# Performance work log

Measured on AMD Instinct MI355X. Metric: run time of the kernel, lower is better.

Reference implementation:

```python
import jax, jax.numpy as jnp
from jax import lax
import numpy as np

HEAD_DIM = 64

def _conv(x, w, stride, pad, groups=1):
    return lax.conv_general_dilated(x, w, (stride, stride), ((pad, pad), (pad, pad)),
                                    dimension_numbers=('NCHW', 'OIHW', 'NCHW'),
                                    feature_group_count=groups)

def _conv_transpose(x, w, b, stride=2, pad=1):
    # PyTorch ConvTranspose2d weight layout is [in, out, kh, kw]
    wf = jnp.transpose(w, (1, 0, 2, 3))[:, :, ::-1, ::-1]
    p = w.shape[2] - 1 - pad
    y = lax.conv_general_dilated(x, wf, (1, 1), ((p, p), (p, p)),
                                 lhs_dilation=(stride, stride),
                                 dimension_numbers=('NCHW', 'OIHW', 'NCHW'))
    return y + b[None, :, None, None]

def _bn(x, g, b, m, v):
    s = g / jnp.sqrt(v + 1e-5)
    return x * s[None, :, None, None] + (b - m * s)[None, :, None, None]

def _relu6(x):
    return jnp.clip(x, 0.0, 6.0)

def reference(x, down_w, down_b, up_w, up_b, coarse_qkv_w, coarse_qkv_b,
              topk_qkv_w, topk_qkv_b, dw_w, bn1_g, bn1_b, bn1_m, bn1_v,
              pw_w, bn2_g, bn2_b, bn2_m, bn2_v):
    hd = HEAD_DIM
    # ---- CoarseSelfAttention ----
    xd = _conv(x, down_w, 2, 1) + down_b[None, :, None, None]   # [B,C,h,w]
    B, C, h, w = xd.shape
    nh = C // hd
    t = xd.reshape(B, nh, hd, h * w).transpose(0, 1, 3, 2)      # [B,nh,hw,hd]
    qkv = t @ coarse_qkv_w.T + coarse_qkv_b
    q, k, v = jnp.split(qkv, 3, axis=-1)
    attn = jax.nn.softmax(jnp.einsum('bnid,bnjd->bnij', k, q), axis=-1)  # k @ q^T (unscaled, as in source)
    coarse_score = attn.sum(axis=-2)                            # [B,nh,hw]
    K = (h * w) // 4
    _, top_k = lax.top_k(coarse_score, K)                       # [B,nh,K]
    out = jnp.einsum('bnij,bnjd->bnid', attn, v)
    out = out.transpose(0, 1, 3, 2).reshape(B, C, h, w)
    coarse_out = _conv_transpose(out, up_w, up_b)               # [B,C,H,W]

    # ---- TopkSelfAttention ----
    H, W = coarse_out.shape[2], coarse_out.shape[3]
    P = (H // 2) * (W // 2)
    xh = coarse_out.reshape(B, nh, hd, H, W)
    # unfold(3,2,2).unfold(4,2,2) -> [B,nh,hd,H/2,W/2,2,2] -> [B,nh,hd,P,2,2]
    patches = xh.reshape(B, nh, hd, H // 2, 2, W // 2, 2).transpose(0, 1, 2, 3, 5, 4, 6)
    patches = patches.reshape(B, nh, hd, P, 2, 2)
    idx = jnp.broadcast_to(top_k[:, :, None, :, None, None], (B, nh, hd, K, 2, 2))
    gathered = jnp.take_along_axis(patches, idx, axis=3)        # [B,nh,hd,K,2,2]
    tokens = gathered.reshape(B, nh, hd, K * 4).transpose(0, 1, 3, 2)  # [B,nh,4K,hd]
    qkv2 = tokens @ topk_qkv_w.T + topk_qkv_b
    q2, k2, v2 = jnp.split(qkv2, 3, axis=-1)
    attn2 = jax.nn.softmax(jnp.einsum('bnid,bnjd->bnij', k2, q2), axis=-1)
    out2 = jnp.einsum('bnij,bnjd->bnid', attn2, v2)             # [B,nh,4K,hd]
    out2 = out2.transpose(0, 1, 3, 2).reshape(B, nh, hd, K, 2, 2)
    bi = jnp.arange(B)[:, None, None]
    hi = jnp.arange(nh)[None, :, None]
    # scatter-add attended patches back into residual patches
    res = patches.at[bi, hi, :, top_k].add(out2.transpose(0, 1, 3, 2, 4, 5))
    # faithful to torch's reshape(batch, -1, patch*2, patch*2) (row-major flatten)
    region = res.reshape(B, C, H, W)

    # ---- residual add + DWConv ----
    y = coarse_out + region
    y = _relu6(_bn(_conv(y, dw_w, 1, 1, groups=C), bn1_g, bn1_b, bn1_m, bn1_v))
    y = _relu6(_bn(_conv(y, pw_w, 1, 0), bn2_g, bn2_b, bn2_m, bn2_v))
    return y

def setup_inputs() -> dict:
    key = jax.random.key(0)
    ks = jax.random.split(key, 20)
    B, C, H, W = 8, 256, 64, 64
    hd = HEAD_DIM
    s = 0.02
    n = jax.random.normal
    inp = {
        'x': n(ks[0], (B, C, H, W), dtype=jnp.float32),
        'down_w': n(ks[1], (C, C, 4, 4), dtype=jnp.float32) * s,
        'down_b': n(ks[2], (C,), dtype=jnp.float32) * s,
        'up_w': n(ks[3], (C, C, 4, 4), dtype=jnp.float32) * s,  # [in,out,kh,kw]
        'up_b': n(ks[4], (C,), dtype=jnp.float32) * s,
        'coarse_qkv_w': n(ks[5], (3 * hd, hd), dtype=jnp.float32) * s,
        'coarse_qkv_b': n(ks[6], (3 * hd,), dtype=jnp.float32) * s,
        'topk_qkv_w': n(ks[7], (3 * hd, hd), dtype=jnp.float32) * s,
        'topk_qkv_b': n(ks[8], (3 * hd,), dtype=jnp.float32) * s,
        'dw_w': n(ks[9], (C, 1, 3, 3), dtype=jnp.float32) * s,
        'bn1_g': 1.0 + n(ks[10], (C,), dtype=jnp.float32) * 0.1,
        'bn1_b': n(ks[11], (C,), dtype=jnp.float32) * 0.1,
        'bn1_m': n(ks[12], (C,), dtype=jnp.float32) * 0.1,
        'bn1_v': jax.random.uniform(ks[13], (C,), dtype=jnp.float32, minval=0.5, maxval=1.5),
        'pw_w': n(ks[14], (C, C, 1, 1), dtype=jnp.float32) * s,
        'bn2_g': 1.0 + n(ks[15], (C,), dtype=jnp.float32) * 0.1,
        'bn2_b': n(ks[16], (C,), dtype=jnp.float32) * 0.1,
        'bn2_m': n(ks[17], (C,), dtype=jnp.float32) * 0.1,
        'bn2_v': jax.random.uniform(ks[18], (C,), dtype=jnp.float32, minval=0.5, maxval=1.5),
    }
    return inp
```

## Files before the change

### kernel.cpp

```cpp
#include <hip/hip_runtime.h>

typedef short short8 __attribute__((ext_vector_type(8)));
typedef float f32x4 __attribute__((ext_vector_type(4)));

__device__ inline unsigned short f32_to_bf16_rne(float f) {
  unsigned int u = __float_as_uint(f);
  unsigned int r = (u + 0x7fffu + ((u >> 16) & 1u)) >> 16;
  return (unsigned short)r;
}
__device__ inline float bf16_to_f32(unsigned short h) {
  return __uint_as_float(((unsigned int)h) << 16);
}

constexpr size_t OFF_XD    = 0;
constexpr size_t OFF_Q     = 2097152;
constexpr size_t OFF_K     = 4194304;
constexpr size_t OFF_V     = 6291456;
constexpr size_t OFF_ATT   = 8388608;
constexpr size_t OFF_SPART = 10485760;
constexpr size_t OFF_SCORE = 14680064;
constexpr size_t OFF_IDX   = 14712832;
constexpr size_t OFF_COUT  = 14721024;
constexpr size_t OFF_Y     = 23109632;
constexpr size_t OFF_T1    = 31498240;
constexpr size_t WS_FLOATS = 39886848;

__global__ __launch_bounds__(256) void k_x2bf(const float* __restrict__ x,
    unsigned short* __restrict__ xbh, unsigned short* __restrict__ xbl) {
  int bid = blockIdx.x;
  int b = bid >> 7;
  int ih = (bid >> 1) & 63;
  int iwh = bid & 1;
  int t = threadIdx.x;
  __shared__ float ts[256][33];
  for (int it = 0; it < 32; ++it) {
    int idx = it * 256 + t;
    int ci = idx >> 5;
    int iwl = idx & 31;
    ts[ci][iwl] = x[(((size_t)(b * 256 + ci) * 64 + ih) * 64) + iwh * 32 + iwl];
  }
  __syncthreads();
  int iwl = t >> 3;
  int cb = (t & 7) * 32;
  size_t base = (((size_t)(b * 64 + ih) * 64) + iwh * 32 + iwl) * 256 + cb;
#pragma unroll
  for (int j = 0; j < 32; j += 2) {
    float v0 = ts[cb + j][iwl];
    float v1 = ts[cb + j + 1][iwl];
    unsigned short h0 = f32_to_bf16_rne(v0);
    unsigned short h1 = f32_to_bf16_rne(v1);
    unsigned short l0 = f32_to_bf16_rne(v0 - bf16_to_f32(h0));
    unsigned short l1 = f32_to_bf16_rne(v1 - bf16_to_f32(h1));
    *(ushort2*)&xbh[base + j] = make_ushort2(h0, h1);
    *(ushort2*)&xbl[base + j] = make_ushort2(l0, l1);
  }
}

__global__ __launch_bounds__(256) void k_wt_dnb(const float* __restrict__ w,
    unsigned short* __restrict__ dwhi, unsigned short* __restrict__ dwlo) {
  int idx = blockIdx.x * 256 + threadIdx.x;
  int ci = idx & 255;
  int co = (idx >> 8) & 255;
  int kk = idx >> 16;
  float v = w[((size_t)(co * 256 + ci)) * 16 + kk];
  unsigned short h = f32_to_bf16_rne(v);
  unsigned short l = f32_to_bf16_rne(v - bf16_to_f32(h));
  dwhi[idx] = h;
  dwlo[idx] = l;
}

__global__ __launch_bounds__(256) void k_wt_upb(const float* __restrict__ w,
    unsigned short* __restrict__ whi, unsigned short* __restrict__ wlo) {
  int idx = blockIdx.x * 256 + threadIdx.x;
  int ci = idx & 255;
  int co = (idx >> 8) & 255;
  int tp = idx >> 16;
  int cls = tp >> 2, tap = tp & 3;
  int r = cls >> 1, s = cls & 1;
  int a_ = tap >> 1, b_ = tap & 1;
  int kh = a_ ? (r ? 2 : 3) : (r ? 0 : 1);
  int kw = b_ ? (s ? 2 : 3) : (s ? 0 : 1);
  float v = w[((size_t)(ci * 256 + co)) * 16 + kh * 4 + kw];
  unsigned short h = f32_to_bf16_rne(v);
  unsigned short l = f32_to_bf16_rne(v - bf16_to_f32(h));
  whi[idx] = h;
  wlo[idx] = l;
}

__global__ __launch_bounds__(256) void k_conv_down_mfma(
    const unsigned short* __restrict__ xbh, const unsigned short* __restrict__ xbl,
    const unsigned short* __restrict__ dwhi, const unsigned short* __restrict__ dwlo,
    const float* __restrict__ bias, float* __restrict__ part) {
  int blk = blockIdx.x;
  int pt = blk & 31;
  int ct = (blk >> 5) & 3;
  int b = (blk >> 7) & 7;
  int ks = blk >> 10;
  int oh2 = pt >> 1;
  int owh = pt & 1;
  int tid = threadIdx.x;
  int w = tid >> 6;
  int lane = tid & 63;
  int lq = lane >> 4;
  int lr = lane & 15;
  int co = ct * 64 + w * 16 + lr;

  __shared__ __align__(16) unsigned short AH[6][34][40];
  __shared__ __align__(16) unsigned short AL[6][34][40];

  f32x4 acc[2];
  acc[0] = (f32x4){0.f, 0.f, 0.f, 0.f};
  acc[1] = (f32x4){0.f, 0.f, 0.f, 0.f};

  int ih0 = 4 * oh2 - 1;
  int iw0 = owh * 32 - 1;
  const short8 zero8 = {0, 0, 0, 0, 0, 0, 0, 0};

  for (int ch = 0; ch < 2; ++ch) {
    int ci0 = ks * 64 + ch * 32;
    __syncthreads();
    for (int idx = tid; idx < 6 * 34 * 4; idx += 256) {
      int q = idx & 3;
      int cell = idx >> 2;
      int row = cell / 34;
      int col = cell - row * 34;
      int ih = ih0 + row;
      int iw = iw0 + col;
      short8 h = zero8, l = zero8;
      if ((unsigned)ih < 64u && (unsigned)iw < 64u) {
        size_t gg = (((size_t)(b * 64 + ih) * 64) + iw) * 256 + ci0 + q * 8;
        h = *(const short8*)&xbh[gg];
        l = *(const short8*)&xbl[gg];
      }
      *(short8*)&AH[row][col][q * 8] = h;
      *(short8*)&AL[row][col][q * 8] = l;
    }
    __syncthreads();
#pragma unroll
    for (int tap = 0; tap < 16; ++tap) {
      int kh = tap >> 2, kw = tap & 3;
      size_t woff = ((size_t)tap * 256 + co) * 256 + ci0 + 8 * lq;
      short8 bh = *(const short8*)&dwhi[woff];
      short8 bl = *(const short8*)&dwlo[woff];
#pragma unroll
      for (int pf = 0; pf < 2; ++pf) {
        short8 ah = *(const short8*)&AH[2 * pf + kh][2 * lr + kw][8 * lq];
        short8 al = *(const short8*)&AL[2 * pf + kh][2 * lr + kw][8 * lq];
        acc[pf] = __builtin_amdgcn_mfma_f32_16x16x32_bf16(ah, bh, acc[pf], 0, 0, 0);
        acc[pf] = __builtin_amdgcn_mfma_f32_16x16x32_bf16(al, bh, acc[pf], 0, 0, 0);
        acc[pf] = __builtin_amdgcn_mfma_f32_16x16x32_bf16(ah, bl, acc[pf], 0, 0, 0);
      }
    }
  }

  float bv = (ks == 0) ? bias[co] : 0.f;
  int bn = b * 4 + ct;
  int d = w * 16 + lr;
  float* pb = part + (size_t)ks * 2097152;
#pragma unroll
  for (int pf = 0; pf < 2; ++pf) {
    int oh = 2 * oh2 + pf;
#pragma unroll
    for (int reg = 0; reg < 4; ++reg) {
      int ow = owh * 16 + lq * 4 + reg;
      int pix = oh * 32 + ow;
      pb[((size_t)bn * 1024 + pix) * 64 + d] = acc[pf][reg] + bv;
    }
  }
}

__global__ __launch_bounds__(192) void k_qkv_coarse(const float* __restrict__ part,
    const float* __restrict__ W, const float* __restrict__ bias,
    unsigned short* __restrict__ qh, unsigned short* __restrict__ ql,
    unsigned short* __restrict__ kh, unsigned short* __restrict__ kl,
    unsigned short* __restrict__ vth, unsigned short* __restrict__ vtl) {
  int blk = blockIdx.x;
  int bn = blk >> 4;
  int i0 = (blk & 15) * 64;
  int tid = threadIdx.x;
  int w = tid >> 6;
  int lane = tid & 63;

  __shared__ __align__(16) char lraw[66560];
  float (*ts)[68] = (float(*)[68])lraw;
  float (*Ws)[64] = (float(*)[64])(lraw + 17408);

  for (int idx = tid; idx < 1024; idx += 192) {
    int row = idx >> 4, c4 = (idx & 15) * 4;
    size_t o = ((size_t)(bn * 1024 + i0 + row)) * 64 + c4;
    float4 v0 = *(const float4*)&part[o];
    float4 v1 = *(const float4*)&part[o + 2097152];
    float4 v2 = *(const float4*)&part[o + 2 * 2097152];
    float4 v3 = *(const float4*)&part[o + 3 * 2097152];
    float4 sv = make_float4(((v0.x + v1.x) + v2.x) + v3.x,
                            ((v0.y + v1.y) + v2.y) + v3.y,
                            ((v0.z + v1.z) + v2.z) + v3.z,
                            ((v0.w + v1.w) + v2.w) + v3.w);
    *(float4*)&ts[row][c4] = sv;
  }
  for (int idx = tid; idx < 3072; idx += 192) {
    int e = idx >> 4, c4 = (idx & 15) * 4;
    *(float4*)&Ws[e][c4] = *(const float4*)&W[(size_t)e * 64 + c4];
  }
  __syncthreads();

  float t[64];
#pragma unroll
  for (int c = 0; c < 16; ++c) {
    float4 v = *(const float4*)&ts[lane][c * 4];
    t[c * 4] = v.x; t[c * 4 + 1] = v.y; t[c * 4 + 2] = v.z; t[c * 4 + 3] = v.w;
  }
  int e0 = w * 64;
  short8 ph[8], pl[8];
#pragma unroll
  for (int ec = 0; ec < 8; ++ec) {
    short8 hh, ll;
#pragma unroll
    for (int k = 0; k < 8; ++k) {
      int e = e0 + ec * 8 + k;
      float acc = bias[e];
#pragma unroll
      for (int d = 0; d < 64; ++d) acc = fmaf(t[d], Ws[e][d], acc);
      unsigned short h = f32_to_bf16_rne(acc);
      hh[k] = (short)h;
      ll[k] = (short)f32_to_bf16_rne(acc - bf16_to_f32(h));
    }
    ph[ec] = hh; pl[ec] = ll;
  }
  __syncthreads();
  unsigned short* outH = (unsigned short*)(lraw + w * 18432);
  unsigned short* outL = (unsigned short*)(lraw + w * 18432 + 9216);
#pragma unroll
  for (int ec = 0; ec < 8; ++ec) {
    *(short8*)&outH[lane * 72 + ec * 8] = ph[ec];
    *(short8*)&outL[lane * 72 + ec * 8] = pl[ec];
  }
  if (w < 2) {
    unsigned short* dh = w ? kh : qh;
    unsigned short* dl = w ? kl : ql;
#pragma unroll
    for (int k = 0; k < 8; ++k) {
      int flat = (lane + k * 64) * 8;
      int row = flat >> 6, d = flat & 63;
      size_t go = ((size_t)(bn * 1024 + i0 + row)) * 64 + d;
      *(short8*)&dh[go] = *(const short8*)&outH[row * 72 + d];
      *(short8*)&dl[go] = *(const short8*)&outL[row * 72 + d];
    }
  } else {
    int db = lane >> 3, i8 = (lane & 7) * 8;
#pragma unroll
    for (int k = 0; k < 8; ++k) {
      int dd = db + k * 8;
      short8 hh, ll;
#pragma unroll
      for (int tt = 0; tt < 8; ++tt) {
        hh[tt] = (short)outH[(i8 + tt) * 72 + dd];
        ll[tt] = (short)outL[(i8 + tt) * 72 + dd];
      }
      size_t go = ((size_t)(bn * 64 + dd)) * 1024 + i0 + i8;
      *(short8*)&vth[go] = hh;
      *(short8*)&vtl[go] = ll;
    }
  }
}

__global__ __launch_bounds__(192) void k_qkv_topk(const float* __restrict__ coutT,
    const int* __restrict__ idxb, const float* __restrict__ W, const float* __restrict__ bias,
    unsigned short* __restrict__ qh, unsigned short* __restrict__ ql,
    unsigned short* __restrict__ kh, unsigned short* __restrict__ kl,
    unsigned short* __restrict__ vth, unsigned short* __restrict__ vtl) {
  int blk = blockIdx.x;
  int bn = blk >> 4;
  int i0 = (blk & 15) * 64;
  int tid = threadIdx.x;
  int w = tid >> 6;
  int lane = tid & 63;

  __shared__ __align__(16) char lraw[66560];
  float (*ts)[68] = (float(*)[68])lraw;
  float (*Ws)[64] = (float(*)[64])(lraw + 17408);
  __shared__ int gs[64];

  if (tid < 64) {
    int row = tid;
    int p = idxb[bn * 256 + ((i0 + row) >> 2)] & 1023;
    int a = (row >> 1) & 1, b = row & 1;
    gs[row] = ((p >> 5) * 2 + a) * 64 + (p & 31) * 2 + b;
  }
  __syncthreads();
  for (int idx = tid; idx < 1024; idx += 192) {
    int row = idx >> 4, c4 = (idx & 15) * 4;
    *(float4*)&ts[row][c4] =
        *(const float4*)&coutT[((size_t)bn * 4096 + gs[row]) * 64 + c4];
  }
  for (int idx = tid; idx < 3072; idx += 192) {
    int e = idx >> 4, c4 = (idx & 15) * 4;
    *(float4*)&Ws[e][c4] = *(const float4*)&W[(size_t)e * 64 + c4];
  }
  __syncthreads();

  float t[64];
#pragma unroll
  for (int c = 0; c < 16; ++c) {
    float4 v = *(const float4*)&ts[lane][c * 4];
    t[c * 4] = v.x; t[c * 4 + 1] = v.y; t[c * 4 + 2] = v.z; t[c * 4 + 3] = v.w;
  }
  int e0 = w * 64;
  short8 ph[8], pl[8];
#pragma unroll
  for (int ec = 0; ec < 8; ++ec) {
    short8 hh, ll;
#pragma unroll
    for (int k = 0; k < 8; ++k) {
      int e = e0 + ec * 8 + k;
      float acc = bias[e];
#pragma unroll
      for (int d = 0; d < 64; ++d) acc = fmaf(t[d], Ws[e][d], acc);
      unsigned short h = f32_to_bf16_rne(acc);
      hh[k] = (short)h;
      ll[k] = (short)f32_to_bf16_rne(acc - bf16_to_f32(h));
    }
    ph[ec] = hh; pl[ec] = ll;
  }
  __syncthreads();
  unsigned short* outH = (unsigned short*)(lraw + w * 18432);
  unsigned short* outL = (unsigned short*)(lraw + w * 18432 + 9216);
#pragma unroll
  for (int ec = 0; ec < 8; ++ec) {
    *(short8*)&outH[lane * 72 + ec * 8] = ph[ec];
    *(short8*)&outL[lane * 72 + ec * 8] = pl[ec];
  }
  if (w < 2) {
    unsigned short* dh = w ? kh : qh;
    unsigned short* dl = w ? kl : ql;
#pragma unroll
    for (int k = 0; k < 8; ++k) {
      int flat = (lane + k * 64) * 8;
      int row = flat >> 6, d = flat & 63;
      size_t go = ((size_t)(bn * 1024 + i0 + row)) * 64 + d;
      *(short8*)&dh[go] = *(const short8*)&outH[row * 72 + d];
      *(short8*)&dl[go] = *(const short8*)&outL[row * 72 + d];
    }
  } else {
    int db = lane >> 3, i8 = (lane & 7) * 8;
#pragma unroll
    for (int k = 0; k < 8; ++k) {
      int dd = db + k * 8;
      short8 hh, ll;
#pragma unroll
      for (int tt = 0; tt < 8; ++tt) {
        hh[tt] = (short)outH[(i8 + tt) * 72 + dd];
        ll[tt] = (short)outL[(i8 + tt) * 72 + dd];
      }
      size_t go = ((size_t)(bn * 64 + dd)) * 1024 + i0 + i8;
      *(short8*)&vth[go] = hh;
      *(short8*)&vtl[go] = ll;
    }
  }
}

__global__ __launch_bounds__(256) void k_attn_score_mfma(
    const unsigned short* __restrict__ qh, const unsigned short* __restrict__ ql,
    const unsigned short* __restrict__ kh, const unsigned short* __restrict__ kl,
    const unsigned short* __restrict__ vth, const unsigned short* __restrict__ vtl,
    float* __restrict__ spart, float* __restrict__ attT) {
  int blk = blockIdx.x;
  int bn = blk & 31;
  int it = blk >> 5;
  int tid = threadIdx.x;
  int w = tid >> 6;
  int lane = tid & 63;
  int g = lane >> 4;
  int c = lane & 15;
  size_t qb = (size_t)bn << 16;

  __shared__ __align__(16) unsigned short QH[64][72];
  __shared__ __align__(16) unsigned short QL[64][72];
  __shared__ __align__(16) unsigned short VH[64][72];
  __shared__ __align__(16) unsigned short VL[64][72];
  __shared__ __align__(16) unsigned short PH[64][72];
  __shared__ __align__(16) unsigned short PL[64][72];
  __shared__ float sacc[1024];
  for (int i2 = tid; i2 < 1024; i2 += 256) sacc[i2] = 0.f;

  int r0 = tid >> 3;
  int c8 = (tid & 7) * 8;

  int irow = it * 64 + w * 16 + c;
  short8 kfh[2], kfl[2];
#pragma unroll
  for (int ch = 0; ch < 2; ++ch) {
    kfh[ch] = *(const short8*)&kh[qb + (size_t)irow * 64 + ch * 32 + g * 8];
    kfl[ch] = *(const short8*)&kl[qb + (size_t)irow * 64 + ch * 32 + g * 8];
  }

  float m[4], lsum[4];
#pragma unroll
  for (int r = 0; r < 4; ++r) { m[r] = -3.0e38f; lsum[r] = 0.f; }

  for (int jt = 0; jt < 16; ++jt) {
    __syncthreads();
#pragma unroll
    for (int rr = 0; rr < 2; ++rr) {
      int row = r0 + rr * 32;
      size_t go = qb + (size_t)(jt * 64 + row) * 64 + c8;
      *(short8*)&QH[row][c8] = *(const short8*)&qh[go];
      *(short8*)&QL[row][c8] = *(const short8*)&ql[go];
    }
    __syncthreads();
    f32x4 s[4];
#pragma unroll
    for (int su = 0; su < 4; ++su) s[su] = (f32x4){0.f, 0.f, 0.f, 0.f};
#pragma unroll
    for (int ch = 0; ch < 2; ++ch)
#pragma unroll
      for (int su = 0; su < 4; ++su) {
        short8 qfh = *(const short8*)&QH[su * 16 + c][ch * 32 + g * 8];
        short8 qfl = *(const short8*)&QL[su * 16 + c][ch * 32 + g * 8];
        s[su] = __builtin_amdgcn_mfma_f32_16x16x32_bf16(kfh[ch], qfh, s[su], 0, 0, 0);
        s[su] = __builtin_amdgcn_mfma_f32_16x16x32_bf16(kfl[ch], qfh, s[su], 0, 0, 0);
        s[su] = __builtin_amdgcn_mfma_f32_16x16x32_bf16(kfh[ch], qfl, s[su], 0, 0, 0);
      }
#pragma unroll
    for (int r = 0; r < 4; ++r) {
      float tm = fmaxf(fmaxf(s[0][r], s[1][r]), fmaxf(s[2][r], s[3][r]));
#pragma unroll
      for (int off = 1; off <= 8; off <<= 1) tm = fmaxf(tm, __shfl_xor(tm, off, 64));
      float mn = fmaxf(m[r], tm);
      float ts = ((expf(s[0][r] - mn) + expf(s[1][r] - mn)) +
                  expf(s[2][r] - mn)) + expf(s[3][r] - mn);
#pragma unroll
      for (int off = 1; off <= 8; off <<= 1) ts += __shfl_xor(ts, off, 64);
      lsum[r] = lsum[r] * expf(m[r] - mn) + ts;
      m[r] = mn;
    }
  }
  float inv[4];
#pragma unroll
  for (int r = 0; r < 4; ++r) inv[r] = 1.f / lsum[r];

  f32x4 oacc[4];
#pragma unroll
  for (int d = 0; d < 4; ++d) oacc[d] = (f32x4){0.f, 0.f, 0.f, 0.f};

  for (int jt = 0; jt < 16; ++jt) {
    __syncthreads();
#pragma unroll
    for (int rr = 0; rr < 2; ++rr) {
      int row = r0 + rr * 32;
      size_t go = qb + (size_t)(jt * 64 + row) * 64 + c8;
      *(short8*)&QH[row][c8] = *(const short8*)&qh[go];
      *(short8*)&QL[row][c8] = *(const short8*)&ql[go];
      size_t vo = ((size_t)(bn * 64 + row)) * 1024 + jt * 64 + c8;
      *(short8*)&VH[row][c8] = *(const short8*)&vth[vo];
      *(short8*)&VL[row][c8] = *(const short8*)&vtl[vo];
    }
    __syncthreads();
    f32x4 s[4];
#pragma unroll
    for (int su = 0; su < 4; ++su) s[su] = (f32x4){0.f, 0.f, 0.f, 0.f};
#pragma unroll
    for (int ch = 0; ch < 2; ++ch)
#pragma unroll
      for (int su = 0; su < 4; ++su) {
        short8 qfh = *(const short8*)&QH[su * 16 + c][ch * 32 + g * 8];
        short8 qfl = *(const short8*)&QL[su * 16 + c][ch * 32 + g * 8];
        s[su] = __builtin_amdgcn_mfma_f32_16x16x32_bf16(kfh[ch], qfh, s[su], 0, 0, 0);
        s[su] = __builtin_amdgcn_mfma_f32_16x16x32_bf16(kfl[ch], qfh, s[su], 0, 0, 0);
        s[su] = __builtin_amdgcn_mfma_f32_16x16x32_bf16(kfh[ch], qfl, s[su], 0, 0, 0);
      }
#pragma unroll
    for (int su = 0; su < 4; ++su) {
      float p0 = expf(s[su][0] - m[0]) * inv[0];
      float p1 = expf(s[su][1] - m[1]) * inv[1];
      float p2 = expf(s[su][2] - m[2]) * inv[2];
      float p3 = expf(s[su][3] - m[3]) * inv[3];
      float cs = ((p0 + p1) + p2) + p3;
      cs += __shfl_xor(cs, 16, 64);
      cs += __shfl_xor(cs, 32, 64);
      if (g == 0) atomicAdd(&sacc[jt * 64 + su * 16 + c], cs);
      unsigned short h0 = f32_to_bf16_rne(p0);
      unsigned short h1 = f32_to_bf16_rne(p1);
      unsigned short h2 = f32_to_bf16_rne(p2);
      unsigned short h3 = f32_to_bf16_rne(p3);
      PH[w * 16 + g * 4 + 0][su * 16 + c] = h0;
      PH[w * 16 + g * 4 + 1][su * 16 + c] = h1;
      PH[w * 16 + g * 4 + 2][su * 16 + c] = h2;
      PH[w * 16 + g * 4 + 3][su * 16 + c] = h3;
      PL[w * 16 + g * 4 + 0][su * 16 + c] = f32_to_bf16_rne(p0 - bf16_to_f32(h0));
      PL[w * 16 + g * 4 + 1][su * 16 + c] = f32_to_bf16_rne(p1 - bf16_to_f32(h1));
      PL[w * 16 + g * 4 + 2][su * 16 + c] = f32_to_bf16_rne(p2 - bf16_to_f32(h2));
      PL[w * 16 + g * 4 + 3][su * 16 + c] = f32_to_bf16_rne(p3 - bf16_to_f32(h3));
    }
#pragma unroll
    for (int ch = 0; ch < 2; ++ch) {
      short8 pfh = *(const short8*)&PH[w * 16 + c][ch * 32 + g * 8];
      short8 pfl = *(const short8*)&PL[w * 16 + c][ch * 32 + g * 8];
#pragma unroll
      for (int d = 0; d < 4; ++d) {
        short8 vfh = *(const short8*)&VH[d * 16 + c][ch * 32 + g * 8];
        short8 vfl = *(const short8*)&VL[d * 16 + c][ch * 32 + g * 8];
        oacc[d] = __builtin_amdgcn_mfma_f32_16x16x32_bf16(vfh, pfh, oacc[d], 0, 0, 0);
        oacc[d] = __builtin_amdgcn_mfma_f32_16x16x32_bf16(vfl, pfh, oacc[d], 0, 0, 0);
        oacc[d] = __builtin_amdgcn_mfma_f32_16x16x32_bf16(vfh, pfl, oacc[d], 0, 0, 0);
      }
    }
  }
#pragma unroll
  for (int d = 0; d < 4; ++d)
#pragma unroll
    for (int r = 0; r < 4; ++r)
      attT[((size_t)bn * 64 + d * 16 + g * 4 + r) * 1024 + it * 64 + w * 16 + c] =
          oacc[d][r];
  __syncthreads();
  for (int i2 = tid; i2 < 1024; i2 += 256)
    spart[((size_t)bn * 16 + it) * 1024 + i2] = sacc[i2];
}

__global__ __launch_bounds__(256) void k_attn_online_mfma(
    const unsigned short* __restrict__ qh, const unsigned short* __restrict__ ql,
    const unsigned short* __restrict__ kh, const unsigned short* __restrict__ kl,
    const unsigned short* __restrict__ vth, const unsigned short* __restrict__ vtl,
    float* __restrict__ O) {
  int blk = blockIdx.x;
  int bn = blk & 31;
  int it = blk >> 5;
  int tid = threadIdx.x;
  int w = tid >> 6;
  int lane = tid & 63;
  int g = lane >> 4;
  int c = lane & 15;
  size_t qb = (size_t)bn << 16;

  __shared__ __align__(16) unsigned short QH[64][72];
  __shared__ __align__(16) unsigned short QL[64][72];
  __shared__ __align__(16) unsigned short VH[64][72];
  __shared__ __align__(16) unsigned short VL[64][72];
  __shared__ __align__(16) unsigned short PH[64][72];
  __shared__ __align__(16) unsigned short PL[64][72];

  int r0 = tid >> 3;
  int c8 = (tid & 7) * 8;

  int irow = it * 64 + w * 16 + c;
  short8 kfh[2], kfl[2];
#pragma unroll
  for (int ch = 0; ch < 2; ++ch) {
    kfh[ch] = *(const short8*)&kh[qb + (size_t)irow * 64 + ch * 32 + g * 8];
    kfl[ch] = *(const short8*)&kl[qb + (size_t)irow * 64 + ch * 32 + g * 8];
  }

  float m[4], lsum[4];
  f32x4 oacc[4];
#pragma unroll
  for (int r = 0; r < 4; ++r) { m[r] = -3.0e38f; lsum[r] = 0.f; }
#pragma unroll
  for (int d = 0; d < 4; ++d) oacc[d] = (f32x4){0.f, 0.f, 0.f, 0.f};

  for (int jt = 0; jt < 16; ++jt) {
    __syncthreads();
#pragma unroll
    for (int rr = 0; rr < 2; ++rr) {
      int row = r0 + rr * 32;
      size_t go = qb + (size_t)(jt * 64 + row) * 64 + c8;
      *(short8*)&QH[row][c8] = *(const short8*)&qh[go];
      *(short8*)&QL[row][c8] = *(const short8*)&ql[go];
      size_t vo = ((size_t)(bn * 64 + row)) * 1024 + jt * 64 + c8;
      *(short8*)&VH[row][c8] = *(const short8*)&vth[vo];
      *(short8*)&VL[row][c8] = *(const short8*)&vtl[vo];
    }
    __syncthreads();
    f32x4 s[4];
#pragma unroll
    for (int su = 0; su < 4; ++su) s[su] = (f32x4){0.f, 0.f, 0.f, 0.f};
#pragma unroll
    for (int ch = 0; ch < 2; ++ch)
#pragma unroll
      for (int su = 0; su < 4; ++su) {
        short8 qfh = *(const short8*)&QH[su * 16 + c][ch * 32 + g * 8];
        short8 qfl = *(const short8*)&QL[su * 16 + c][ch * 32 + g * 8];
        s[su] = __builtin_amdgcn_mfma_f32_16x16x32_bf16(kfh[ch], qfh, s[su], 0, 0, 0);
        s[su] = __builtin_amdgcn_mfma_f32_16x16x32_bf16(kfl[ch], qfh, s[su], 0, 0, 0);
        s[su] = __builtin_amdgcn_mfma_f32_16x16x32_bf16(kfh[ch], qfl, s[su], 0, 0, 0);
      }
    float sc[4];
#pragma unroll
    for (int r = 0; r < 4; ++r) {
      float tm = fmaxf(fmaxf(s[0][r], s[1][r]), fmaxf(s[2][r], s[3][r]));
#pragma unroll
      for (int off = 1; off <= 8; off <<= 1) tm = fmaxf(tm, __shfl_xor(tm, off, 64));
      float mn = fmaxf(m[r], tm);
      sc[r] = expf(m[r] - mn);
      float p0 = expf(s[0][r] - mn);
      float p1 = expf(s[1][r] - mn);
      float p2 = expf(s[2][r] - mn);
      float p3 = expf(s[3][r] - mn);
      s[0][r] = p0; s[1][r] = p1; s[2][r] = p2; s[3][r] = p3;
      float ts = ((p0 + p1) + p2) + p3;
#pragma unroll
      for (int off = 1; off <= 8; off <<= 1) ts += __shfl_xor(ts, off, 64);
      lsum[r] = lsum[r] * sc[r] + ts;
      m[r] = mn;
    }
#pragma unroll
    for (int su = 0; su < 4; ++su) {
      unsigned short h0 = f32_to_bf16_rne(s[su][0]);
      unsigned short h1 = f32_to_bf16_rne(s[su][1]);
      unsigned short h2 = f32_to_bf16_rne(s[su][2]);
      unsigned short h3 = f32_to_bf16_rne(s[su][3]);
      PH[w * 16 + g * 4 + 0][su * 16 + c] = h0;
      PH[w * 16 + g * 4 + 1][su * 16 + c] = h1;
      PH[w * 16 + g * 4 + 2][su * 16 + c] = h2;
      PH[w * 16 + g * 4 + 3][su * 16 + c] = h3;
      PL[w * 16 + g * 4 + 0][su * 16 + c] = f32_to_bf16_rne(s[su][0] - bf16_to_f32(h0));
      PL[w * 16 + g * 4 + 1][su * 16 + c] = f32_to_bf16_rne(s[su][1] - bf16_to_f32(h1));
      PL[w * 16 + g * 4 + 2][su * 16 + c] = f32_to_bf16_rne(s[su][2] - bf16_to_f32(h2));
      PL[w * 16 + g * 4 + 3][su * 16 + c] = f32_to_bf16_rne(s[su][3] - bf16_to_f32(h3));
    }
    float s01 = (c & 1) ? sc[1] : sc[0];
    float s23 = (c & 1) ? sc[3] : sc[2];
    float tmp = (c & 2) ? s23 : s01;
    float scc = __shfl(tmp, ((c >> 2) << 4) | c, 64);
#pragma unroll
    for (int d = 0; d < 4; ++d) oacc[d] *= scc;
#pragma unroll
    for (int ch = 0; ch < 2; ++ch) {
      short8 pfh = *(const short8*)&PH[w * 16 + c][ch * 32 + g * 8];
      short8 pfl = *(const short8*)&PL[w * 16 + c][ch * 32 + g * 8];
#pragma unroll
      for (int d = 0; d < 4; ++d) {
        short8 vfh = *(const short8*)&VH[d * 16 + c][ch * 32 + g * 8];
        short8 vfl = *(const short8*)&VL[d * 16 + c][ch * 32 + g * 8];
        oacc[d] = __builtin_amdgcn_mfma_f32_16x16x32_bf16(vfh, pfh, oacc[d], 0, 0, 0);
        oacc[d] = __builtin_amdgcn_mfma_f32_16x16x32_bf16(vfl, pfh, oacc[d], 0, 0, 0);
        oacc[d] = __builtin_amdgcn_mfma_f32_16x16x32_bf16(vfh, pfl, oacc[d], 0, 0, 0);
      }
    }
  }
  float i01 = (c & 1) ? (1.f / lsum[1]) : (1.f / lsum[0]);
  float i23 = (c & 1) ? (1.f / lsum[3]) : (1.f / lsum[2]);
  float itmp = (c & 2) ? i23 : i01;
  float invc = __shfl(itmp, ((c >> 2) << 4) | c, 64);
#pragma unroll
  for (int d = 0; d < 4; ++d) {
    f32x4 o4 = oacc[d] * invc;
    *(f32x4*)&O[((size_t)bn * 1024 + it * 64 + w * 16 + c) * 64 + d * 16 + g * 4] = o4;
  }
}

__global__ __launch_bounds__(256) void k_score_reduce(const float* __restrict__ part,
                                                      float* __restrict__ score) {
  int j = blockIdx.x * 256 + threadIdx.x;
  int bn = j >> 10, jj = j & 1023;
  float s = 0.f;
  for (int g = 0; g < 16; ++g) s += part[((size_t)bn * 16 + g) * 1024 + jj];
  score[j] = s;
}

__global__ __launch_bounds__(256) void k_idx_init(int* __restrict__ idx) {
  int j = blockIdx.x * 256 + threadIdx.x;
  idx[j] = j & 255;
}

__global__ __launch_bounds__(1024) void k_topk(const float* __restrict__ score,
                                               int* __restrict__ idxout) {
  int bn = blockIdx.x;
  int t = threadIdx.x;
  __shared__ float s[1024];
  s[t] = score[bn * 1024 + t];
  __syncthreads();
  float my = s[t];
  int rank = 0;
  for (int j = 0; j < 1024; ++j) {
    float o = s[j];
    rank += (o > my) || (o == my && j < t);
  }
  if (rank < 256) idxout[bn * 256 + rank] = t;
}

__global__ __launch_bounds__(256) void k_conv_up_mfma(
    const float* __restrict__ attT, const unsigned short* __restrict__ whi,
    const unsigned short* __restrict__ wlo, const float* __restrict__ bias,
    float* __restrict__ cout, float* __restrict__ coutT) {
  int blk = blockIdx.x;
  int ct = blk & 3;
  int pt = (blk >> 2) & 15;
  int cls = (blk >> 6) & 3;
  int b = blk >> 8;
  int r = cls >> 1, s = cls & 1;
  int Ib = pt * 2;
  int co0 = ct * 64;
  int tid = threadIdx.x;
  int w = tid >> 6;
  int lane = tid & 63;
  int lq = lane >> 4;
  int lr = lane & 15;
  int wr = w >> 1;
  int wc = w & 1;
  int co0w = co0 + wc * 32;

  __shared__ __align__(16) unsigned short AH[3][33][40];
  __shared__ __align__(16) unsigned short AL[3][33][40];

  f32x4 acc[2][2];
#pragma unroll
  for (int pf = 0; pf < 2; ++pf)
#pragma unroll
    for (int cf = 0; cf < 2; ++cf) acc[pf][cf] = (f32x4){0.f, 0.f, 0.f, 0.f};

  const float* ab = attT + (size_t)b * 4 * 65536;
  int ih_base = Ib + r - 1;
  int iw_base = s - 1;

  for (int ci0 = 0; ci0 < 256; ci0 += 32) {
    int n = ci0 >> 6, d0 = ci0 & 63;
    __syncthreads();
    for (int idx = tid; idx < 3168; idx += 256) {
      int ciL = idx / 99;
      int rem = idx - ciL * 99;
      int rho = rem / 33;
      int c = rem - rho * 33;
      int ih = ih_base + rho;
      int iw = iw_base + c;
      float v = 0.f;
      if ((unsigned)ih < 32u && (unsigned)iw < 32u)
        v = ab[((size_t)n * 64 + d0 + ciL) * 1024 + ih * 32 + iw];
      unsigned short h = f32_to_bf16_rne(v);
      unsigned short lo = f32_to_bf16_rne(v - bf16_to_f32(h));
      AH[rho][c][ciL] = h;
      AL[rho][c][ciL] = lo;
    }
    __syncthreads();
#pragma unroll
    for (int tap = 0; tap < 4; ++tap) {
      int a_ = tap >> 1, b_ = tap & 1;
      int rho = wr + 1 - a_;
      short8 ah[2], al[2];
#pragma unroll
      for (int pf = 0; pf < 2; ++pf) {
        int col = pf * 16 + lr + 1 - b_;
        ah[pf] = *(const short8*)&AH[rho][col][8 * lq];
        al[pf] = *(const short8*)&AL[rho][col][8 * lq];
      }
      size_t wb = (size_t)(cls * 4 + tap) * 65536;
      short8 bh[2], bl[2];
#pragma unroll
      for (int cf = 0; cf < 2; ++cf) {
        size_t off = wb + (size_t)(co0w + cf * 16 + lr) * 256 + ci0 + 8 * lq;
        bh[cf] = *(const short8*)&whi[off];
        bl[cf] = *(const short8*)&wlo[off];
      }
#pragma unroll
      for (int pf = 0; pf < 2; ++pf)
#pragma unroll
        for (int cf = 0; cf < 2; ++cf) {
          acc[pf][cf] = __builtin_amdgcn_mfma_f32_16x16x32_bf16(ah[pf], bh[cf], acc[pf][cf], 0, 0, 0);
          acc[pf][cf] = __builtin_amdgcn_mfma_f32_16x16x32_bf16(al[pf], bh[cf], acc[pf][cf], 0, 0, 0);
          acc[pf][cf] = __builtin_amdgcn_mfma_f32_16x16x32_bf16(ah[pf], bl[cf], acc[pf][cf], 0, 0, 0);
        }
    }
  }

  int I = Ib + wr;
  int oh = 2 * I + r;
#pragma unroll
  for (int pf = 0; pf < 2; ++pf)
#pragma unroll
    for (int cf = 0; cf < 2; ++cf) {
      int co = co0w + cf * 16 + lr;
      float bv = bias[co];
      size_t cbase = ((size_t)b * 256 + co) * 4096 + oh * 64;
      size_t tbase = ((size_t)(b * 4 + (co >> 6)) * 4096 + oh * 64);
#pragma unroll
      for (int qd = 0; qd < 4; ++qd) {
        int J = pf * 16 + lq * 4 + qd;
        int ow = 2 * J + s;
        float val = acc[pf][cf][qd] + bv;
        cout[cbase + ow] = val;
        coutT[(tbase + ow) * 64 + (co & 63)] = val;
      }
    }
}

__global__ __launch_bounds__(256) void k_ybuild(const float* __restrict__ cout,
                                                float* __restrict__ y) {
  size_t e = (size_t)blockIdx.x * 256 + threadIdx.x;
  int flat = (int)(e & 4095);
  size_t bc = e >> 12;
  int p = flat >> 2, ab = flat & 3;
  int a = ab >> 1, bi = ab & 1;
  int src = ((p >> 5) * 2 + a) * 64 + (p & 31) * 2 + bi;
  const float* cb = cout + bc * 4096;
  y[e] = cb[flat] + cb[src];
}

__global__ __launch_bounds__(256) void k_scatter(const float* __restrict__ out2,
    const int* __restrict__ idx, float* __restrict__ y) {
  int e = blockIdx.x * 256 + threadIdx.x;
  int d = e & 63;
  int r = e >> 6;
  int ab = r & 3;
  int r2 = r >> 2;
  int kk = r2 & 255;
  int bn = r2 >> 8;
  int b = bn >> 2, n = bn & 3;
  int p = idx[bn * 256 + kk] & 1023;
  int flat = p * 4 + ab;
  int t = kk * 4 + ab;
  y[((size_t)(b * 256 + n * 64 + d)) * 4096 + flat] +=
      out2[((size_t)bn * 1024 + t) * 64 + d];
}

__global__ __launch_bounds__(256) void k_dw(const float* __restrict__ y,
    const float* __restrict__ w, const float* __restrict__ g, const float* __restrict__ bb,
    const float* __restrict__ mm, const float* __restrict__ vv, float* __restrict__ t1) {
  size_t e = (size_t)blockIdx.x * 256 + threadIdx.x;
  int pix = (int)(e & 4095);
  int c = (int)((e >> 12) & 255);
  int oh = pix >> 6, ow = pix & 63;
  const float* yb = y + (e - pix);
  float acc = 0.f;
#pragma unroll
  for (int kh = 0; kh < 3; ++kh) {
    int ih = oh - 1 + kh;
    if ((unsigned)ih >= 64u) continue;
#pragma unroll
    for (int kw = 0; kw < 3; ++kw) {
      int iw = ow - 1 + kw;
      if ((unsigned)iw >= 64u) continue;
      acc = fmaf(yb[ih * 64 + iw], w[c * 9 + kh * 3 + kw], acc);
    }
  }
  float s = g[c] * rsqrtf(vv[c] + 1e-5f);
  float val = acc * s + (bb[c] - mm[c] * s);
  t1[e] = fminf(fmaxf(val, 0.f), 6.f);
}

__global__ __launch_bounds__(256) void k_pw2(const float* __restrict__ t1,
    const float* __restrict__ w, const float* __restrict__ g, const float* __restrict__ bb,
    const float* __restrict__ mm, const float* __restrict__ vv, float* __restrict__ out) {
  int blk = blockIdx.x;
  int tile = blk & 3;
  int cog = (blk >> 2) & 63;
  int b = blk >> 8;
  int co0 = cog * 4;
  int t = threadIdx.x;
  __shared__ float wl[256][4];
  for (int idx = t; idx < 1024; idx += 256) {
    int cof = idx >> 8;
    int ci = idx & 255;
    wl[ci][cof] = w[(co0 + cof) * 256 + ci];
  }
  __syncthreads();
  int px0 = tile * 1024 + t * 4;
  const float* tb = t1 + (size_t)b * 256 * 4096 + px0;
  float acc[4][4];
#pragma unroll
  for (int a = 0; a < 4; ++a)
#pragma unroll
    for (int jj = 0; jj < 4; ++jj) acc[a][jj] = 0.f;
  for (int ci = 0; ci < 256; ++ci) {
    float4 tv = *(const float4*)(tb + (size_t)ci * 4096);
    float4 wv = *(const float4*)&wl[ci][0];
    acc[0][0] = fmaf(tv.x, wv.x, acc[0][0]); acc[0][1] = fmaf(tv.y, wv.x, acc[0][1]);
    acc[0][2] = fmaf(tv.z, wv.x, acc[0][2]); acc[0][3] = fmaf(tv.w, wv.x, acc[0][3]);
    acc[1][0] = fmaf(tv.x, wv.y, acc[1][0]); acc[1][1] = fmaf(tv.y, wv.y, acc[1][1]);
    acc[1][2] = fmaf(tv.z, wv.y, acc[1][2]); acc[1][3] = fmaf(tv.w, wv.y, acc[1][3]);
    acc[2][0] = fmaf(tv.x, wv.z, acc[2][0]); acc[2][1] = fmaf(tv.y, wv.z, acc[2][1]);
    acc[2][2] = fmaf(tv.z, wv.z, acc[2][2]); acc[2][3] = fmaf(tv.w, wv.z, acc[2][3]);
    acc[3][0] = fmaf(tv.x, wv.w, acc[3][0]); acc[3][1] = fmaf(tv.y, wv.w, acc[3][1]);
    acc[3][2] = fmaf(tv.z, wv.w, acc[3][2]); acc[3][3] = fmaf(tv.w, wv.w, acc[3][3]);
  }
#pragma unroll
  for (int a = 0; a < 4; ++a) {
    int co = co0 + a;
    float s = g[co] * rsqrtf(vv[co] + 1e-5f);
    float bias = bb[co] - mm[co] * s;
    float4 o4;
    o4.x = fminf(fmaxf(acc[a][0] * s + bias, 0.f), 6.f);
    o4.y = fminf(fmaxf(acc[a][1] * s + bias, 0.f), 6.f);
    o4.z = fminf(fmaxf(acc[a][2] * s + bias, 0.f), 6.f);
    o4.w = fminf(fmaxf(acc[a][3] * s + bias, 0.f), 6.f);
    *(float4*)(out + ((size_t)(b * 256 + co)) * 4096 + px0) = o4;
  }
}

extern "C" void kernel_launch(void* const* d_in, const int* in_sizes, int n_in,
                              void* d_out, int out_size, void* d_ws, size_t ws_size,
                              hipStream_t stream) {
  if (ws_size < WS_FLOATS * sizeof(float)) return;

  const float* x      = (const float*)d_in[0];
  const float* down_w = (const float*)d_in[1];
  const float* down_b = (const float*)d_in[2];
  const float* up_w   = (const float*)d_in[3];
  const float* up_b   = (const float*)d_in[4];
  const float* cqkv_w = (const float*)d_in[5];
  const float* cqkv_b = (const float*)d_in[6];
  const float* tqkv_w = (const float*)d_in[7];
  const float* tqkv_b = (const float*)d_in[8];
  const float* dww    = (const float*)d_in[9];
  const float* bn1g   = (const float*)d_in[10];
  const float* bn1b   = (const float*)d_in[11];
  const float* bn1m   = (const float*)d_in[12];
  const float* bn1v   = (const float*)d_in[13];
  const float* pww    = (const float*)d_in[14];
  const float* bn2g   = (const float*)d_in[15];
  const float* bn2b   = (const float*)d_in[16];
  const float* bn2m   = (const float*)d_in[17];
  const float* bn2v   = (const float*)d_in[18];

  float* ws    = (float*)d_ws;
  float* att   = ws + OFF_ATT;
  float* spart = ws + OFF_SPART;
  float* score = ws + OFF_SCORE;
  int*   idx   = (int*)(ws + OFF_IDX);
  float* cout  = ws + OFF_COUT;
  float* y     = ws + OFF_Y;
  float* t1    = ws + OFF_T1;
  float* attT  = ws + OFF_SPART + 2097152;
  unsigned short* whi  = (unsigned short*)(ws + OFF_XD);
  unsigned short* wlo  = (unsigned short*)(ws + OFF_XD + 524288);
  unsigned short* dwhi = (unsigned short*)(ws + OFF_SPART);
  unsigned short* dwlo = (unsigned short*)(ws + OFF_SPART + 524288);
  unsigned short* xbh  = (unsigned short*)(ws + OFF_Q);
  unsigned short* xbl  = (unsigned short*)(ws + OFF_V);
  unsigned short* qh   = (unsigned short*)(ws + OFF_Q);
  unsigned short* ql   = (unsigned short*)(ws + OFF_Q + 1048576);
  unsigned short* kh   = (unsigned short*)(ws + OFF_K);
  unsigned short* kl   = (unsigned short*)(ws + OFF_K + 1048576);
  unsigned short* vth  = (unsigned short*)(ws + OFF_V);
  unsigned short* vtl  = (unsigned short*)(ws + OFF_V + 1048576);
  float* coutT = ws + OFF_T1;
  float* dpart = ws + OFF_Y;

  k_x2bf<<<1024, 256, 0, stream>>>(x, xbh, xbl);
  k_wt_dnb<<<4096, 256, 0, stream>>>(down_w, dwhi, dwlo);
  k_conv_down_mfma<<<4096, 256, 0, stream>>>(xbh, xbl, dwhi, dwlo, down_b, dpart);
  k_qkv_coarse<<<512, 192, 0, stream>>>(dpart, cqkv_w, cqkv_b, qh, ql, kh, kl, vth, vtl);
  k_wt_upb<<<4096, 256, 0, stream>>>(up_w, whi, wlo);
  k_attn_score_mfma<<<512, 256, 0, stream>>>(qh, ql, kh, kl, vth, vtl, spart, attT);
  k_score_reduce<<<128, 256, 0, stream>>>(spart, score);
  k_idx_init<<<32, 256, 0, stream>>>(idx);
  k_topk<<<32, 1024, 0, stream>>>(score, idx);
  k_conv_up_mfma<<<2048, 256, 0, stream>>>(attT, whi, wlo, up_b, cout, coutT);
  k_qkv_topk<<<512, 192, 0, stream>>>(coutT, idx, tqkv_w, tqkv_b, qh, ql, kh, kl, vth, vtl);
  k_attn_online_mfma<<<512, 256, 0, stream>>>(qh, ql, kh, kl, vth, vtl, att);
  k_ybuild<<<32768, 256, 0, stream>>>(cout, y);
  k_scatter<<<8192, 256, 0, stream>>>(att, idx, y);
  k_dw<<<32768, 256, 0, stream>>>(y, dww, bn1g, bn1b, bn1m, bn1v, t1);
  k_pw2<<<2048, 256, 0, stream>>>(t1, pww, bn2g, bn2b, bn2m, bn2v, (float*)d_out);
}
```

Before: 927.8 us.

## Retile transposed conv to cover both column parities per block; pre-split attention to bf16

The attention-score kernel now writes its output directly as bf16 hi/lo pairs instead of fp32, so the up-conv no longer redoes the split for every loaded element. The up-conv kernel is retiled: each block handles one input row and one row parity for all 256 output channels and both column parities. This reuses the shared-memory input tile across more MFMAs, cuts the grid from 2048 to 512 blocks, and lets cout be written with float2 stores. In exchange each block holds a larger accumulator array (32 f32x4), which raises register pressure and may lower occupancy.

```diff
diff --git a/kernel.cpp b/kernel.cpp
--- a/kernel.cpp
+++ b/kernel.cpp
@@ -363,7 +363,8 @@
     const unsigned short* __restrict__ qh, const unsigned short* __restrict__ ql,
     const unsigned short* __restrict__ kh, const unsigned short* __restrict__ kl,
     const unsigned short* __restrict__ vth, const unsigned short* __restrict__ vtl,
-    float* __restrict__ spart, float* __restrict__ attT) {
+    float* __restrict__ spart, unsigned short* __restrict__ atth,
+    unsigned short* __restrict__ attl) {
   int blk = blockIdx.x;
   int bn = blk & 31;
   int it = blk >> 5;
@@ -509,9 +510,14 @@
 #pragma unroll
   for (int d = 0; d < 4; ++d)
 #pragma unroll
-    for (int r = 0; r < 4; ++r)
-      attT[((size_t)bn * 64 + d * 16 + g * 4 + r) * 1024 + it * 64 + w * 16 + c] =
-          oacc[d][r];
+    for (int r = 0; r < 4; ++r) {
+      float v = oacc[d][r];
+      unsigned short h = f32_to_bf16_rne(v);
+      unsigned short l = f32_to_bf16_rne(v - bf16_to_f32(h));
+      size_t o = ((size_t)bn * 64 + d * 16 + g * 4 + r) * 1024 + it * 64 + w * 16 + c;
+      atth[o] = h;
+      attl[o] = l;
+    }
   __syncthreads();
   for (int i2 = tid; i2 < 1024; i2 += 256)
     spart[((size_t)bn * 16 + it) * 1024 + i2] = sacc[i2];
@@ -679,107 +685,107 @@
 }
 
 __global__ __launch_bounds__(256) void k_conv_up_mfma(
-    const float* __restrict__ attT, const unsigned short* __restrict__ whi,
-    const unsigned short* __restrict__ wlo, const float* __restrict__ bias,
-    float* __restrict__ cout, float* __restrict__ coutT) {
+    const unsigned short* __restrict__ atth, const unsigned short* __restrict__ attl,
+    const unsigned short* __restrict__ whi, const unsigned short* __restrict__ wlo,
+    const float* __restrict__ bias, float* __restrict__ cout,
+    float* __restrict__ coutT) {
   int blk = blockIdx.x;
-  int ct = blk & 3;
-  int pt = (blk >> 2) & 15;
-  int cls = (blk >> 6) & 3;
-  int b = blk >> 8;
-  int r = cls >> 1, s = cls & 1;
-  int Ib = pt * 2;
-  int co0 = ct * 64;
+  int I = blk & 31;
+  int r = (blk >> 5) & 1;
+  int b = blk >> 6;
   int tid = threadIdx.x;
   int w = tid >> 6;
   int lane = tid & 63;
   int lq = lane >> 4;
   int lr = lane & 15;
-  int wr = w >> 1;
-  int wc = w & 1;
-  int co0w = co0 + wc * 32;
-
-  __shared__ __align__(16) unsigned short AH[3][33][40];
-  __shared__ __align__(16) unsigned short AL[3][33][40];
-
-  f32x4 acc[2][2];
-#pragma unroll
-  for (int pf = 0; pf < 2; ++pf)
-#pragma unroll
-    for (int cf = 0; cf < 2; ++cf) acc[pf][cf] = (f32x4){0.f, 0.f, 0.f, 0.f};
-
-  const float* ab = attT + (size_t)b * 4 * 65536;
-  int ih_base = Ib + r - 1;
-  int iw_base = s - 1;
+
+  __shared__ __align__(16) unsigned short AH[2][34][40];
+  __shared__ __align__(16) unsigned short AL[2][34][40];
+
+  f32x4 acc[2][2][4];
+#pragma unroll
+  for (int s = 0; s < 2; ++s)
+#pragma unroll
+    for (int pf = 0; pf < 2; ++pf)
+#pragma unroll
+      for (int cf = 0; cf < 4; ++cf) acc[s][pf][cf] = (f32x4){0.f, 0.f, 0.f, 0.f};
+
+  const unsigned short* abh = atth + (size_t)b * 262144;
+  const unsigned short* abl = attl + (size_t)b * 262144;
+  int ih0 = I + r - 1;
 
   for (int ci0 = 0; ci0 < 256; ci0 += 32) {
     int n = ci0 >> 6, d0 = ci0 & 63;
     __syncthreads();
-    for (int idx = tid; idx < 3168; idx += 256) {
-      int ciL = idx / 99;
-      int rem = idx - ciL * 99;
-      int rho = rem / 33;
-      int c = rem - rho * 33;
-      int ih = ih_base + rho;
-      int iw = iw_base + c;
-      float v = 0.f;
-      if ((unsigned)ih < 32u && (unsigned)iw < 32u)
-        v = ab[((size_t)n * 64 + d0 + ciL) * 1024 + ih * 32 + iw];
-      unsigned short h = f32_to_bf16_rne(v);
-      unsigned short lo = f32_to_bf16_rne(v - bf16_to_f32(h));
-      AH[rho][c][ciL] = h;
-      AL[rho][c][ciL] = lo;
+    for (int idx = tid; idx < 2176; idx += 256) {
+      int cr = idx / 34;
+      int col = idx - cr * 34;
+      int ciL = cr >> 1, rho = cr & 1;
+      int ih = ih0 + rho;
+      int iw = col - 1;
+      unsigned short h = 0, l = 0;
+      if ((unsigned)ih < 32u && (unsigned)iw < 32u) {
+        size_t gg = ((size_t)(n * 64 + d0 + ciL)) * 1024 + ih * 32 + iw;
+        h = abh[gg];
+        l = abl[gg];
+      }
+      AH[rho][col][ciL] = h;
+      AL[rho][col][ciL] = l;
     }
     __syncthreads();
 #pragma unroll
     for (int tap = 0; tap < 4; ++tap) {
       int a_ = tap >> 1, b_ = tap & 1;
-      int rho = wr + 1 - a_;
-      short8 ah[2], al[2];
-#pragma unroll
-      for (int pf = 0; pf < 2; ++pf) {
-        int col = pf * 16 + lr + 1 - b_;
-        ah[pf] = *(const short8*)&AH[rho][col][8 * lq];
-        al[pf] = *(const short8*)&AL[rho][col][8 * lq];
-      }
-      size_t wb = (size_t)(cls * 4 + tap) * 65536;
-      short8 bh[2], bl[2];
-#pragma unroll
-      for (int cf = 0; cf < 2; ++cf) {
-        size_t off = wb + (size_t)(co0w + cf * 16 + lr) * 256 + ci0 + 8 * lq;
-        bh[cf] = *(const short8*)&whi[off];
-        bl[cf] = *(const short8*)&wlo[off];
-      }
-#pragma unroll
-      for (int pf = 0; pf < 2; ++pf)
-#pragma unroll
-        for (int cf = 0; cf < 2; ++cf) {
-          acc[pf][cf] = __builtin_amdgcn_mfma_f32_16x16x32_bf16(ah[pf], bh[cf], acc[pf][cf], 0, 0, 0);
-          acc[pf][cf] = __builtin_amdgcn_mfma_f32_16x16x32_bf16(al[pf], bh[cf], acc[pf][cf], 0, 0, 0);
-          acc[pf][cf] = __builtin_amdgcn_mfma_f32_16x16x32_bf16(ah[pf], bl[cf], acc[pf][cf], 0, 0, 0);
+      int rho = 1 - a_;
+#pragma unroll
+      for (int s = 0; s < 2; ++s) {
+        int cls = r * 2 + s;
+        size_t wb = (size_t)(cls * 4 + tap) * 65536;
+        short8 bh[4], bl[4];
+#pragma unroll
+        for (int cf = 0; cf < 4; ++cf) {
+          size_t off = wb + (size_t)(w * 64 + cf * 16 + lr) * 256 + ci0 + 8 * lq;
+          bh[cf] = *(const short8*)&whi[off];
+          bl[cf] = *(const short8*)&wlo[off];
         }
-    }
-  }
-
-  int I = Ib + wr;
+        short8 ah[2], al[2];
+#pragma unroll
+        for (int pf = 0; pf < 2; ++pf) {
+          int col = pf * 16 + lr + s - b_ + 1;
+          ah[pf] = *(const short8*)&AH[rho][col][8 * lq];
+          al[pf] = *(const short8*)&AL[rho][col][8 * lq];
+        }
+#pragma unroll
+        for (int pf = 0; pf < 2; ++pf)
+#pragma unroll
+          for (int cf = 0; cf < 4; ++cf) {
+            acc[s][pf][cf] = __builtin_amdgcn_mfma_f32_16x16x32_bf16(ah[pf], bh[cf], acc[s][pf][cf], 0, 0, 0);
+            acc[s][pf][cf] = __builtin_amdgcn_mfma_f32_16x16x32_bf16(al[pf], bh[cf], acc[s][pf][cf], 0, 0, 0);
+            acc[s][pf][cf] = __builtin_amdgcn_mfma_f32_16x16x32_bf16(ah[pf], bl[cf], acc[s][pf][cf], 0, 0, 0);
+          }
+      }
+    }
+  }
+
   int oh = 2 * I + r;
 #pragma unroll
-  for (int pf = 0; pf < 2; ++pf)
-#pragma unroll
-    for (int cf = 0; cf < 2; ++cf) {
-      int co = co0w + cf * 16 + lr;
-      float bv = bias[co];
-      size_t cbase = ((size_t)b * 256 + co) * 4096 + oh * 64;
-      size_t tbase = ((size_t)(b * 4 + (co >> 6)) * 4096 + oh * 64);
-#pragma unroll
-      for (int qd = 0; qd < 4; ++qd) {
-        int J = pf * 16 + lq * 4 + qd;
-        int ow = 2 * J + s;
-        float val = acc[pf][cf][qd] + bv;
-        cout[cbase + ow] = val;
-        coutT[(tbase + ow) * 64 + (co & 63)] = val;
-      }
-    }
+  for (int cf = 0; cf < 4; ++cf) {
+    int co = w * 64 + cf * 16 + lr;
+    float bv = bias[co];
+    size_t cbase = ((size_t)b * 256 + co) * 4096 + (size_t)oh * 64;
+    size_t tbase = (((size_t)(b * 4 + w) * 4096) + oh * 64) * 64 + (co & 63);
+#pragma unroll
+    for (int pf = 0; pf < 2; ++pf)
+#pragma unroll
+      for (int reg = 0; reg < 4; ++reg) {
+        int J = pf * 16 + lq * 4 + reg;
+        float v0 = acc[0][pf][cf][reg] + bv;
+        float v1 = acc[1][pf][cf][reg] + bv;
+        *(float2*)&cout[cbase + 2 * J] = make_float2(v0, v1);
+        coutT[tbase + (size_t)(2 * J) * 64] = v0;
+        coutT[tbase + (size_t)(2 * J + 1) * 64] = v1;
+      }
+  }
 }
 
 __global__ __launch_bounds__(256) void k_ybuild(const float* __restrict__ cout,
@@ -918,7 +924,8 @@
   float* cout  = ws + OFF_COUT;
   float* y     = ws + OFF_Y;
   float* t1    = ws + OFF_T1;
-  float* attT  = ws + OFF_SPART + 2097152;
+  unsigned short* atth = (unsigned short*)(ws + OFF_SPART + 2097152);
+  unsigned short* attl = (unsigned short*)(ws + OFF_SPART + 3145728);
   unsigned short* whi  = (unsigned short*)(ws + OFF_XD);
   unsigned short* wlo  = (unsigned short*)(ws + OFF_XD + 524288);
   unsigned short* dwhi = (unsigned short*)(ws + OFF_SPART);
@@ -939,11 +946,11 @@
   k_conv_down_mfma<<<4096, 256, 0, stream>>>(xbh, xbl, dwhi, dwlo, down_b, dpart);
   k_qkv_coarse<<<512, 192, 0, stream>>>(dpart, cqkv_w, cqkv_b, qh, ql, kh, kl, vth, vtl);
   k_wt_upb<<<4096, 256, 0, stream>>>(up_w, whi, wlo);
-  k_attn_score_mfma<<<512, 256, 0, stream>>>(qh, ql, kh, kl, vth, vtl, spart, attT);
+  k_attn_score_mfma<<<512, 256, 0, stream>>>(qh, ql, kh, kl, vth, vtl, spart, atth, attl);
   k_score_reduce<<<128, 256, 0, stream>>>(spart, score);
   k_idx_init<<<32, 256, 0, stream>>>(idx);
   k_topk<<<32, 1024, 0, stream>>>(score, idx);
-  k_conv_up_mfma<<<2048, 256, 0, stream>>>(attT, whi, wlo, up_b, cout, coutT);
+  k_conv_up_mfma<<<512, 256, 0, stream>>>(atth, attl, whi, wlo, up_b, cout, coutT);
   k_qkv_topk<<<512, 192, 0, stream>>>(coutT, idx, tqkv_w, tqkv_b, qh, ql, kh, kl, vth, vtl);
   k_attn_online_mfma<<<512, 256, 0, stream>>>(qh, ql, kh, kl, vth, vtl, att);
   k_ybuild<<<32768, 256, 0, stream>>>(cout, y);
```

Measured after the change: 890.8 us. 1.04x faster.
